# Kernel optimization log

Measured on AMD Instinct MI355X. Metric: run time of the kernel, lower is better.

The kernel has to match this reference:

```python
import jax, jax.numpy as jnp
import numpy as np

B, C, T, H, W = 4, 16, 32, 64, 64
KD = 2  # key_dim == value_dim == 2 (hard-coded by reshape in original)


def setup_inputs() -> dict:
    key = jax.random.key(0)
    k0, k1, k2, k3, k4 = jax.random.split(key, 5)
    hw = H * W
    x = jax.random.uniform(k0, (B, C, T, H, W), dtype=jnp.float32)
    # positive weights keep v and out_s*out_t positive so sqrt stays real
    w_qkv_s = jax.random.uniform(k1, (3 * KD, T), dtype=jnp.float32) * (2.0 / T)
    w_qkv_t = jax.random.uniform(k2, (3 * KD, hw), dtype=jnp.float32) * (2.0 / hw)
    w_out_s = jax.random.uniform(k3, (C, C * KD), dtype=jnp.float32) * (2.0 / (C * KD))
    w_out_t = jax.random.uniform(k4, (C, C * KD), dtype=jnp.float32) * (2.0 / (C * KD))
    return {"x": x, "w_qkv_s": w_qkv_s, "w_qkv_t": w_qkv_t,
            "w_out_s": w_out_s, "w_out_t": w_out_t}


def reference(x, w_qkv_s, w_qkv_t, w_out_s, w_out_t):
    b, c, t, h, w = x.shape
    hw = h * w
    # spatial qkv: 1x1 conv over time-as-channel -> (b,c,3*KD,hw)
    qkv_s = jnp.einsum('bcthw,kt->bckhw', x, w_qkv_s).reshape(b, c, 3 * KD, hw)
    qs, ks, vs = qkv_s[:, :, :KD], qkv_s[:, :, KD:2 * KD], qkv_s[:, :, 2 * KD:]
    # temporal qkv: 1x1 conv over space-as-channel -> (b,c,3*KD,t)
    x_flat = x.reshape(b, c, t, hw)
    qkv_t = jnp.einsum('bctn,kn->bckt', x_flat, w_qkv_t)
    qt, kt, vt = qkv_t[:, :, :KD], qkv_t[:, :, KD:2 * KD], qkv_t[:, :, 2 * KD:]

    qs = jax.nn.softmax(qs, axis=2)[:, :, :, None, :]   # (b,c,KD,1,hw)
    qt = jax.nn.softmax(qt, axis=2)[..., None]          # (b,c,KD,t,1)
    ks = jax.nn.softmax(ks, axis=-1)[:, :, :, None, :]  # (b,c,KD,1,hw)
    kt = jax.nn.softmax(kt, axis=-1)[..., None]         # (b,c,KD,t,1)
    vs = vs[:, :, :, None, :]
    vt = vt[..., None]

    eps = 1e-10
    scale = KD ** (-0.25)
    # log-space geometric mean of spatial and temporal maps -> (b,c,KD,t,hw)
    k = jnp.exp((jnp.log(kt + eps) + jnp.log(ks + eps)) * 0.5) * scale
    q = jnp.exp((jnp.log(qt + eps) + jnp.log(qs + eps)) * 0.5) * scale
    v = jnp.sqrt(vt * vs)

    context = jnp.einsum('bcdtn,bcetn->bcde', k, v)      # (b,c,KD,KD)
    out = jnp.einsum('bcdtn,bcde->bcetn', q, context)    # (b,c,KD,t,hw)
    out = out.reshape(b, c * KD, t, h, w)                # foldTime

    out_s = jnp.einsum('bkthw,ck->bcthw', out, w_out_s)
    out_t = jnp.einsum('bkthw,ck->bcthw', out, w_out_t)
    return jnp.sqrt(out_s * out_t)
```

## Files before the change

kernel.cpp:

```cpp
#include <hip/hip_runtime.h>

#define BB 4
#define CC 16
#define TT 32
#define HWN 4096
#define NCH1 16

#define WS_BQ   0
#define WS_QTP  (WS_BQ + BB*CC*2*HWN)
#define WS_KSP  (WS_QTP + BB*CC*NCH1*192)
#define WS_AQ   (WS_KSP + BB*CC*NCH1*8)
#define WS_CTX  (WS_AQ + BB*CC*2*TT)
#define WS_CST  (WS_CTX + BB*CC*2*2)

__device__ __forceinline__ float wsum64(float v){
#pragma unroll
  for (int m = 1; m < 64; m <<= 1) v += __shfl_xor(v, m, 64);
  return v;
}
__device__ __forceinline__ float wmax64(float v){
#pragma unroll
  for (int m = 1; m < 64; m <<= 1) v = fmaxf(v, __shfl_xor(v, m, 64));
  return v;
}
__device__ __forceinline__ float qsum4(float v){
  int a = __builtin_amdgcn_update_dpp(0, __float_as_int(v), 0xB1, 0xF, 0xF, true);
  float r = v + __int_as_float(a);
  int b = __builtin_amdgcn_update_dpp(0, __float_as_int(r), 0x4E, 0xF, 0xF, true);
  return r + __int_as_float(b);
}

__global__ __launch_bounds__(256) void k1_stage(const float* __restrict__ x,
    const float* __restrict__ wqs, const float* __restrict__ wqt,
    float* __restrict__ ws)
{
  const int bx = blockIdx.x;
  const int ch = bx & 15;
  const int c  = (bx >> 4) & 15;
  const int b  = bx >> 8;
  const int tid  = threadIdx.x;
  const int wave = tid >> 6;
  const int lane = tid & 63;
  const int wave_u = __builtin_amdgcn_readfirstlane(wave);

  __shared__ float4 sacc[4][64][6];
  __shared__ float  qred[4*836];

  const int n0 = ch*256 + lane*4;
  const float* xrow = x + (((size_t)(b*CC + c))*TT + wave_u*8)*(size_t)HWN + n0;

  float4 wt4[6];
#pragma unroll
  for (int k = 0; k < 6; ++k)
    wt4[k] = *(const float4*)(wqt + k*HWN + n0);

  float wq[6][8];
#pragma unroll
  for (int k = 0; k < 6; ++k)
#pragma unroll
    for (int tl = 0; tl < 8; ++tl)
      wq[k][tl] = wqs[k*TT + wave_u*8 + tl];

  float acc[6][4];
  float qt[6][8];
#pragma unroll
  for (int k = 0; k < 6; ++k){
#pragma unroll
    for (int j = 0; j < 4; ++j) acc[k][j] = 0.f;
#pragma unroll
    for (int tl = 0; tl < 8; ++tl) qt[k][tl] = 0.f;
  }

  float4 xv = *(const float4*)(xrow);
#pragma unroll
  for (int tl = 0; tl < 8; ++tl){
    float4 nxt = xv;
    if (tl < 7) nxt = *(const float4*)(xrow + (size_t)(tl+1)*HWN);
#pragma unroll
    for (int k = 0; k < 6; ++k){
      const float w = wq[k][tl];
      acc[k][0] = fmaf(xv.x, w, acc[k][0]);
      acc[k][1] = fmaf(xv.y, w, acc[k][1]);
      acc[k][2] = fmaf(xv.z, w, acc[k][2]);
      acc[k][3] = fmaf(xv.w, w, acc[k][3]);
      float p = qt[k][tl];
      p = fmaf(xv.x, wt4[k].x, p);
      p = fmaf(xv.y, wt4[k].y, p);
      p = fmaf(xv.z, wt4[k].z, p);
      p = fmaf(xv.w, wt4[k].w, p);
      qt[k][tl] = p;
    }
    xv = nxt;
  }

#pragma unroll
  for (int k = 0; k < 6; ++k)
#pragma unroll
    for (int tl = 0; tl < 8; ++tl)
      qt[k][tl] = qsum4(qt[k][tl]);
  if ((lane & 3) == 0){
    float* qp = &qred[wave*836 + (lane >> 2)*52];
#pragma unroll
    for (int k = 0; k < 6; ++k){
      *(float4*)(qp + k*8)     = make_float4(qt[k][0],qt[k][1],qt[k][2],qt[k][3]);
      *(float4*)(qp + k*8 + 4) = make_float4(qt[k][4],qt[k][5],qt[k][6],qt[k][7]);
    }
  }

#pragma unroll
  for (int k = 0; k < 6; ++k)
    sacc[wave][lane][k] = make_float4(acc[k][0], acc[k][1], acc[k][2], acc[k][3]);
  __syncthreads();

  const float eps = 1e-10f;

  if (tid < 192){
    const int k = tid >> 5, t = tid & 31, w = t >> 3, tl = t & 7;
    const float* qp = &qred[w*836 + k*8 + tl];
    float s = 0.f;
#pragma unroll
    for (int g = 0; g < 16; ++g) s += qp[g*52];
    ws[WS_QTP + ((size_t)((b*CC+c)*NCH1 + ch))*192 + tid] = s;
  }

  if (wave == 0){
    float4 s0 = sacc[0][lane][0], s1 = sacc[0][lane][1];
#pragma unroll
    for (int w = 1; w < 4; ++w){
      float4 a = sacc[w][lane][0], bq_ = sacc[w][lane][1];
      s0.x += a.x; s0.y += a.y; s0.z += a.z; s0.w += a.w;
      s1.x += bq_.x; s1.y += bq_.y; s1.z += bq_.z; s1.w += bq_.w;
    }
    float q0[4] = {s0.x, s0.y, s0.z, s0.w};
    float q1[4] = {s1.x, s1.y, s1.z, s1.w};
    float o0[4], o1[4];
#pragma unroll
    for (int j = 0; j < 4; ++j){
      float mm = fmaxf(q0[j], q1[j]);
      float e0 = __expf(q0[j]-mm), e1 = __expf(q1[j]-mm);
      float inv = 1.f/(e0+e1);
      o0[j] = sqrtf(e0*inv + eps);
      o1[j] = sqrtf(e1*inv + eps);
    }
    float* bqp = ws + WS_BQ + ((size_t)((b*CC+c)*2))*HWN + n0;
    *(float4*)(bqp)       = make_float4(o0[0],o0[1],o0[2],o0[3]);
    *(float4*)(bqp + HWN) = make_float4(o1[0],o1[1],o1[2],o1[3]);
  } else if (wave == 1){
    float4 ks0 = sacc[0][lane][2], ks1 = sacc[0][lane][3];
    float4 vs0 = sacc[0][lane][4], vs1 = sacc[0][lane][5];
#pragma unroll
    for (int w = 1; w < 4; ++w){
      float4 a = sacc[w][lane][2], bb = sacc[w][lane][3];
      float4 cc2 = sacc[w][lane][4], dd = sacc[w][lane][5];
      ks0.x += a.x; ks0.y += a.y; ks0.z += a.z; ks0.w += a.w;
      ks1.x += bb.x; ks1.y += bb.y; ks1.z += bb.z; ks1.w += bb.w;
      vs0.x += cc2.x; vs0.y += cc2.y; vs0.z += cc2.z; vs0.w += cc2.w;
      vs1.x += dd.x; vs1.y += dd.y; vs1.z += dd.z; vs1.w += dd.w;
    }
    float k0a[4] = {ks0.x,ks0.y,ks0.z,ks0.w};
    float k1a[4] = {ks1.x,ks1.y,ks1.z,ks1.w};
    float v0a[4] = {vs0.x,vs0.y,vs0.z,vs0.w};
    float v1a[4] = {vs1.x,vs1.y,vs1.z,vs1.w};
    float m0 = fmaxf(fmaxf(k0a[0],k0a[1]), fmaxf(k0a[2],k0a[3]));
    float m1 = fmaxf(fmaxf(k1a[0],k1a[1]), fmaxf(k1a[2],k1a[3]));
    m0 = wmax64(m0); m1 = wmax64(m1);
    float z0=0,z1=0,t00=0,t01=0,t10=0,t11=0;
#pragma unroll
    for (int j = 0; j < 4; ++j){
      float e0 = __expf(k0a[j]-m0);
      float e1 = __expf(k1a[j]-m1);
      z0 += e0; z1 += e1;
      float s0 = sqrtf(e0), s1 = sqrtf(e1);
      float v0 = sqrtf(v0a[j]), v1 = sqrtf(v1a[j]);
      t00 = fmaf(s0, v0, t00);
      t01 = fmaf(s1, v0, t01);
      t10 = fmaf(s0, v1, t10);
      t11 = fmaf(s1, v1, t11);
    }
    z0 = wsum64(z0); z1 = wsum64(z1);
    t00 = wsum64(t00); t01 = wsum64(t01); t10 = wsum64(t10); t11 = wsum64(t11);
    if (lane == 0){
      float* sp = ws + WS_KSP + ((size_t)((b*CC+c)*NCH1 + ch))*8;
      sp[0]=m0; sp[1]=m1; sp[2]=z0; sp[3]=z1;
      sp[4]=t00; sp[5]=t01; sp[6]=t10; sp[7]=t11;
    }
  }
}

__global__ __launch_bounds__(64) void k2_combine(float* __restrict__ ws)
{
  const int bc_ = blockIdx.x;
  const int tid = threadIdx.x;
  __shared__ float qt[192];
  const float eps = 1e-10f;
  const float scale = 0.8408964152537145f;

  for (int i = tid; i < 192; i += 64){
    float s = 0.f;
#pragma unroll
    for (int ch = 0; ch < NCH1; ++ch)
      s += ws[WS_QTP + ((size_t)(bc_*NCH1 + ch))*192 + i];
    qt[i] = s;
  }
  __syncthreads();

  if (tid < TT){
    const int t = tid;
    float q0 = qt[0*TT+t], q1 = qt[1*TT+t];
    float mm = fmaxf(q0,q1);
    float e0 = __expf(q0-mm), e1 = __expf(q1-mm);
    float inv = 1.f/(e0+e1);
    ws[WS_AQ + (bc_*2+0)*TT + t] = sqrtf(e0*inv + eps);
    ws[WS_AQ + (bc_*2+1)*TT + t] = sqrtf(e1*inv + eps);
  }
  if (tid < 2){
    const int d = tid;
    float M = -1e30f;
    for (int t = 0; t < TT; ++t) M = fmaxf(M, qt[(2+d)*TT+t]);
    float Z = 0.f;
    for (int t = 0; t < TT; ++t) Z += __expf(qt[(2+d)*TT+t]-M);
    const float invZ = 1.f/Z;
    float St0 = 0.f, St1 = 0.f;
    for (int t = 0; t < TT; ++t){
      float p = __expf(qt[(2+d)*TT+t]-M)*invZ;
      float r = sqrtf(p + eps);
      St0 += r*sqrtf(qt[4*TT+t]);
      St1 += r*sqrtf(qt[5*TT+t]);
    }
    const float* kp = ws + WS_KSP + (size_t)bc_*NCH1*8;
    float M2 = -1e30f;
    for (int ch = 0; ch < NCH1; ++ch) M2 = fmaxf(M2, kp[ch*8+d]);
    float Z2 = 0.f, Sn0 = 0.f, Sn1 = 0.f;
    for (int ch = 0; ch < NCH1; ++ch){
      const float mc = kp[ch*8+d];
      Z2  += kp[ch*8+2+d]*__expf(mc-M2);
      const float hw = __expf((mc-M2)*0.5f);
      Sn0 += kp[ch*8+4+d]*hw;
      Sn1 += kp[ch*8+6+d]*hw;
    }
    const float invsZ = rsqrtf(Z2);
    Sn0 *= invsZ; Sn1 *= invsZ;
    ws[WS_CTX + (bc_*2+d)*2+0] = scale*St0*Sn0;
    ws[WS_CTX + (bc_*2+d)*2+1] = scale*St1*Sn1;
  }
}

__global__ __launch_bounds__(64) void k3_cs(const float* __restrict__ wos,
    const float* __restrict__ wot, float* __restrict__ ws)
{
  const int bx = blockIdx.x;
  const int b = bx >> 5, t = bx & 31;
  const int tid = threadIdx.x;
  const int mat = tid >> 5, m = tid & 31;
  const int cp = m >> 1, d = m & 1;
  const float scale = 0.8408964152537145f;

  const float aq = ws[WS_AQ + ((size_t)((b*CC+cp)*2+d))*TT + t];
  const float c0 = ws[WS_CTX + ((b*CC+cp)*2+d)*2 + 0];
  const float c1 = ws[WS_CTX + ((b*CC+cp)*2+d)*2 + 1];
  const float a0 = scale*aq*c0, a1 = scale*aq*c1;
  const float* wmat = mat ? wot : wos;
  float vals[16];
#pragma unroll
  for (int c = 0; c < CC; ++c)
    vals[c] = fmaf(wmat[c*32 + cp*2], a0, wmat[c*32 + cp*2 + 1]*a1);
  float* dst = ws + WS_CST + (((size_t)(b*TT+t)*32 + m)*2 + mat)*16;
#pragma unroll
  for (int g = 0; g < 4; ++g)
    *(float4*)(dst + g*4) = make_float4(vals[g*4],vals[g*4+1],vals[g*4+2],vals[g*4+3]);
}

#define FMA4(acc, s, v) { acc.x = fmaf(s, v.x, acc.x); acc.y = fmaf(s, v.y, acc.y); \
                          acc.z = fmaf(s, v.z, acc.z); acc.w = fmaf(s, v.w, acc.w); }

__global__ __launch_bounds__(256) void k4_out(const float* __restrict__ ws,
    float* __restrict__ out)
{
  const int bx = blockIdx.x;
  const int nch  = bx & 3;
  const int half = (bx >> 2) & 1;
  const int t    = (bx >> 3) & (TT-1);
  const int b    = bx >> 8;
  const int tid  = threadIdx.x;

  const int n0 = nch*1024 + tid*4;
  const float* bqbase = ws + WS_BQ + ((size_t)(b*CC*2))*HWN + n0;
  const float* cst = ws + WS_CST + ((size_t)(b*TT+t))*1024 + half*8;

  float4 aS[8], aT[8];
#pragma unroll
  for (int c = 0; c < 8; ++c){
    aS[c] = make_float4(0,0,0,0);
    aT[c] = make_float4(0,0,0,0);
  }

#pragma unroll 4
  for (int m = 0; m < 32; ++m){
    const float4 bq = *(const float4*)(bqbase + (size_t)m*HWN);
    const float* cm = cst + m*32;
    const float4 cs0 = *(const float4*)(cm);
    const float4 cs1 = *(const float4*)(cm + 4);
    const float4 ct0 = *(const float4*)(cm + 16);
    const float4 ct1 = *(const float4*)(cm + 20);
    FMA4(aS[0], cs0.x, bq); FMA4(aS[1], cs0.y, bq);
    FMA4(aS[2], cs0.z, bq); FMA4(aS[3], cs0.w, bq);
    FMA4(aS[4], cs1.x, bq); FMA4(aS[5], cs1.y, bq);
    FMA4(aS[6], cs1.z, bq); FMA4(aS[7], cs1.w, bq);
    FMA4(aT[0], ct0.x, bq); FMA4(aT[1], ct0.y, bq);
    FMA4(aT[2], ct0.z, bq); FMA4(aT[3], ct0.w, bq);
    FMA4(aT[4], ct1.x, bq); FMA4(aT[5], ct1.y, bq);
    FMA4(aT[6], ct1.z, bq); FMA4(aT[7], ct1.w, bq);
  }

  float* outp = out + (((size_t)(b*CC + half*8))*TT + t)*HWN + n0;
#pragma unroll
  for (int c = 0; c < 8; ++c){
    float4 y;
    y.x = sqrtf(aS[c].x*aT[c].x);
    y.y = sqrtf(aS[c].y*aT[c].y);
    y.z = sqrtf(aS[c].z*aT[c].z);
    y.w = sqrtf(aS[c].w*aT[c].w);
    *(float4*)(outp + (size_t)c*TT*HWN) = y;
  }
}

extern "C" void kernel_launch(void* const* d_in, const int* in_sizes, int n_in,
                              void* d_out, int out_size, void* d_ws, size_t ws_size,
                              hipStream_t stream)
{
  const float* x   = (const float*)d_in[0];
  const float* wqs = (const float*)d_in[1];
  const float* wqt = (const float*)d_in[2];
  const float* wos = (const float*)d_in[3];
  const float* wot = (const float*)d_in[4];
  float* out = (float*)d_out;
  float* ws  = (float*)d_ws;

  hipLaunchKernelGGL(k1_stage, dim3(BB*CC*NCH1), dim3(256), 0, stream, x, wqs, wqt, ws);
  hipLaunchKernelGGL(k2_combine, dim3(BB*CC), dim3(64), 0, stream, ws);
  hipLaunchKernelGGL(k3_cs, dim3(BB*TT), dim3(64), 0, stream, wos, wot, ws);
  hipLaunchKernelGGL(k4_out, dim3(BB*TT*8), dim3(256), 0, stream, ws, out);
}
```

Before: 120.0 us.

## Fuse combine and coefficient kernels, halve per-thread width in output kernel

Merges the k2 combine and k3 coefficient kernels into one per-batch kernel that keeps intermediates (aq, context, output weights) in shared memory, saving a launch and a global round-trip. The output kernel now computes two pixels per thread instead of four, doubling the grid to 2048 blocks for more parallelism and lower register pressure. The fused kernel runs only 4 blocks, so its serial work per block grows, and the narrower output kernel reloads the coefficient table twice as often.

```diff
diff --git a/kernel.cpp b/kernel.cpp
--- a/kernel.cpp
+++ b/kernel.cpp
@@ -9,9 +9,7 @@
 #define WS_BQ   0
 #define WS_QTP  (WS_BQ + BB*CC*2*HWN)
 #define WS_KSP  (WS_QTP + BB*CC*NCH1*192)
-#define WS_AQ   (WS_KSP + BB*CC*NCH1*8)
-#define WS_CTX  (WS_AQ + BB*CC*2*TT)
-#define WS_CST  (WS_CTX + BB*CC*2*2)
+#define WS_CST  (WS_KSP + BB*CC*NCH1*8)
 
 __device__ __forceinline__ float wsum64(float v){
 #pragma unroll
@@ -187,47 +185,56 @@
   }
 }
 
-__global__ __launch_bounds__(64) void k2_combine(float* __restrict__ ws)
+__global__ __launch_bounds__(256) void k23_combine(const float* __restrict__ wos,
+    const float* __restrict__ wot, float* __restrict__ ws)
 {
-  const int bc_ = blockIdx.x;
+  const int b = blockIdx.x;
   const int tid = threadIdx.x;
-  __shared__ float qt[192];
+  __shared__ float qt_all[16][192];
+  __shared__ float aq[16][2][32];
+  __shared__ float ctxs[16][2][2];
+  __shared__ float wo[2][512];
   const float eps = 1e-10f;
-  const float scale = 0.8408964152537145f;
-
-  for (int i = tid; i < 192; i += 64){
+  const float scale2 = 0.7071067811865476f;
+
+  for (int i = tid; i < 512; i += 256){
+    wo[0][i] = wos[i];
+    wo[1][i] = wot[i];
+  }
+  for (int i = tid; i < 3072; i += 256){
+    const int c = i / 192, j = i - c*192;
+    const float* qp = ws + WS_QTP + ((size_t)((b*CC+c)*NCH1))*192 + j;
     float s = 0.f;
 #pragma unroll
-    for (int ch = 0; ch < NCH1; ++ch)
-      s += ws[WS_QTP + ((size_t)(bc_*NCH1 + ch))*192 + i];
-    qt[i] = s;
+    for (int ch = 0; ch < NCH1; ++ch) s += qp[ch*192];
+    qt_all[c][j] = s;
   }
   __syncthreads();
 
-  if (tid < TT){
-    const int t = tid;
-    float q0 = qt[0*TT+t], q1 = qt[1*TT+t];
+  for (int i = tid; i < 512; i += 256){
+    const int c = i >> 5, t = i & 31;
+    float q0 = qt_all[c][t], q1 = qt_all[c][32+t];
     float mm = fmaxf(q0,q1);
     float e0 = __expf(q0-mm), e1 = __expf(q1-mm);
     float inv = 1.f/(e0+e1);
-    ws[WS_AQ + (bc_*2+0)*TT + t] = sqrtf(e0*inv + eps);
-    ws[WS_AQ + (bc_*2+1)*TT + t] = sqrtf(e1*inv + eps);
-  }
-  if (tid < 2){
-    const int d = tid;
+    aq[c][0][t] = sqrtf(e0*inv + eps);
+    aq[c][1][t] = sqrtf(e1*inv + eps);
+  }
+  if (tid < 32){
+    const int c = tid >> 1, d = tid & 1;
+    const float* kt = &qt_all[c][(2+d)*32];
     float M = -1e30f;
-    for (int t = 0; t < TT; ++t) M = fmaxf(M, qt[(2+d)*TT+t]);
+    for (int t = 0; t < TT; ++t) M = fmaxf(M, kt[t]);
     float Z = 0.f;
-    for (int t = 0; t < TT; ++t) Z += __expf(qt[(2+d)*TT+t]-M);
+    for (int t = 0; t < TT; ++t) Z += __expf(kt[t]-M);
     const float invZ = 1.f/Z;
     float St0 = 0.f, St1 = 0.f;
     for (int t = 0; t < TT; ++t){
-      float p = __expf(qt[(2+d)*TT+t]-M)*invZ;
-      float r = sqrtf(p + eps);
-      St0 += r*sqrtf(qt[4*TT+t]);
-      St1 += r*sqrtf(qt[5*TT+t]);
-    }
-    const float* kp = ws + WS_KSP + (size_t)bc_*NCH1*8;
+      float r = sqrtf(__expf(kt[t]-M)*invZ + eps);
+      St0 += r*sqrtf(qt_all[c][128+t]);
+      St1 += r*sqrtf(qt_all[c][160+t]);
+    }
+    const float* kp = ws + WS_KSP + ((size_t)(b*CC+c))*NCH1*8;
     float M2 = -1e30f;
     for (int ch = 0; ch < NCH1; ++ch) M2 = fmaxf(M2, kp[ch*8+d]);
     float Z2 = 0.f, Sn0 = 0.f, Sn1 = 0.f;
@@ -239,88 +246,75 @@
       Sn1 += kp[ch*8+6+d]*hw;
     }
     const float invsZ = rsqrtf(Z2);
-    Sn0 *= invsZ; Sn1 *= invsZ;
-    ws[WS_CTX + (bc_*2+d)*2+0] = scale*St0*Sn0;
-    ws[WS_CTX + (bc_*2+d)*2+1] = scale*St1*Sn1;
-  }
-}
-
-__global__ __launch_bounds__(64) void k3_cs(const float* __restrict__ wos,
-    const float* __restrict__ wot, float* __restrict__ ws)
-{
-  const int bx = blockIdx.x;
-  const int b = bx >> 5, t = bx & 31;
-  const int tid = threadIdx.x;
-  const int mat = tid >> 5, m = tid & 31;
-  const int cp = m >> 1, d = m & 1;
-  const float scale = 0.8408964152537145f;
-
-  const float aq = ws[WS_AQ + ((size_t)((b*CC+cp)*2+d))*TT + t];
-  const float c0 = ws[WS_CTX + ((b*CC+cp)*2+d)*2 + 0];
-  const float c1 = ws[WS_CTX + ((b*CC+cp)*2+d)*2 + 1];
-  const float a0 = scale*aq*c0, a1 = scale*aq*c1;
-  const float* wmat = mat ? wot : wos;
-  float vals[16];
-#pragma unroll
-  for (int c = 0; c < CC; ++c)
-    vals[c] = fmaf(wmat[c*32 + cp*2], a0, wmat[c*32 + cp*2 + 1]*a1);
-  float* dst = ws + WS_CST + (((size_t)(b*TT+t)*32 + m)*2 + mat)*16;
-#pragma unroll
-  for (int g = 0; g < 4; ++g)
-    *(float4*)(dst + g*4) = make_float4(vals[g*4],vals[g*4+1],vals[g*4+2],vals[g*4+3]);
-}
-
-#define FMA4(acc, s, v) { acc.x = fmaf(s, v.x, acc.x); acc.y = fmaf(s, v.y, acc.y); \
-                          acc.z = fmaf(s, v.z, acc.z); acc.w = fmaf(s, v.w, acc.w); }
+    ctxs[c][d][0] = scale2*St0*Sn0*invsZ;
+    ctxs[c][d][1] = scale2*St1*Sn1*invsZ;
+  }
+  __syncthreads();
+
+  for (int i = tid; i < 2048; i += 256){
+    const int t = i >> 6, rem = i & 63, mat = rem >> 5, m = rem & 31;
+    const int cp = m >> 1, d = m & 1;
+    const float a  = aq[cp][d][t];
+    const float a0 = a*ctxs[cp][d][0], a1 = a*ctxs[cp][d][1];
+    float vals[16];
+#pragma unroll
+    for (int c = 0; c < CC; ++c)
+      vals[c] = fmaf(wo[mat][c*32 + cp*2], a0, wo[mat][c*32 + cp*2 + 1]*a1);
+    float* dst = ws + WS_CST + ((size_t)(b*TT+t))*1024 + m*32 + mat*16;
+#pragma unroll
+    for (int g = 0; g < 4; ++g)
+      *(float4*)(dst + g*4) = make_float4(vals[g*4],vals[g*4+1],vals[g*4+2],vals[g*4+3]);
+  }
+}
+
+#define FMA2(acc, s, v) { acc.x = fmaf(s, v.x, acc.x); acc.y = fmaf(s, v.y, acc.y); }
 
 __global__ __launch_bounds__(256) void k4_out(const float* __restrict__ ws,
     float* __restrict__ out)
 {
   const int bx = blockIdx.x;
-  const int nch  = bx & 3;
-  const int half = (bx >> 2) & 1;
-  const int t    = (bx >> 3) & (TT-1);
-  const int b    = bx >> 8;
+  const int nch  = bx & 7;
+  const int half = (bx >> 3) & 1;
+  const int t    = (bx >> 4) & (TT-1);
+  const int b    = bx >> 9;
   const int tid  = threadIdx.x;
 
-  const int n0 = nch*1024 + tid*4;
+  const int n0 = nch*512 + tid*2;
   const float* bqbase = ws + WS_BQ + ((size_t)(b*CC*2))*HWN + n0;
   const float* cst = ws + WS_CST + ((size_t)(b*TT+t))*1024 + half*8;
 
-  float4 aS[8], aT[8];
+  float2 aS[8], aT[8];
 #pragma unroll
   for (int c = 0; c < 8; ++c){
-    aS[c] = make_float4(0,0,0,0);
-    aT[c] = make_float4(0,0,0,0);
-  }
-
-#pragma unroll 4
+    aS[c] = make_float2(0.f,0.f);
+    aT[c] = make_float2(0.f,0.f);
+  }
+
+#pragma unroll 8
   for (int m = 0; m < 32; ++m){
-    const float4 bq = *(const float4*)(bqbase + (size_t)m*HWN);
+    const float2 bq = *(const float2*)(bqbase + (size_t)m*HWN);
     const float* cm = cst + m*32;
     const float4 cs0 = *(const float4*)(cm);
     const float4 cs1 = *(const float4*)(cm + 4);
     const float4 ct0 = *(const float4*)(cm + 16);
     const float4 ct1 = *(const float4*)(cm + 20);
-    FMA4(aS[0], cs0.x, bq); FMA4(aS[1], cs0.y, bq);
-    FMA4(aS[2], cs0.z, bq); FMA4(aS[3], cs0.w, bq);
-    FMA4(aS[4], cs1.x, bq); FMA4(aS[5], cs1.y, bq);
-    FMA4(aS[6], cs1.z, bq); FMA4(aS[7], cs1.w, bq);
-    FMA4(aT[0], ct0.x, bq); FMA4(aT[1], ct0.y, bq);
-    FMA4(aT[2], ct0.z, bq); FMA4(aT[3], ct0.w, bq);
-    FMA4(aT[4], ct1.x, bq); FMA4(aT[5], ct1.y, bq);
-    FMA4(aT[6], ct1.z, bq); FMA4(aT[7], ct1.w, bq);
+    FMA2(aS[0], cs0.x, bq); FMA2(aS[1], cs0.y, bq);
+    FMA2(aS[2], cs0.z, bq); FMA2(aS[3], cs0.w, bq);
+    FMA2(aS[4], cs1.x, bq); FMA2(aS[5], cs1.y, bq);
+    FMA2(aS[6], cs1.z, bq); FMA2(aS[7], cs1.w, bq);
+    FMA2(aT[0], ct0.x, bq); FMA2(aT[1], ct0.y, bq);
+    FMA2(aT[2], ct0.z, bq); FMA2(aT[3], ct0.w, bq);
+    FMA2(aT[4], ct1.x, bq); FMA2(aT[5], ct1.y, bq);
+    FMA2(aT[6], ct1.z, bq); FMA2(aT[7], ct1.w, bq);
   }
 
   float* outp = out + (((size_t)(b*CC + half*8))*TT + t)*HWN + n0;
 #pragma unroll
   for (int c = 0; c < 8; ++c){
-    float4 y;
+    float2 y;
     y.x = sqrtf(aS[c].x*aT[c].x);
     y.y = sqrtf(aS[c].y*aT[c].y);
-    y.z = sqrtf(aS[c].z*aT[c].z);
-    y.w = sqrtf(aS[c].w*aT[c].w);
-    *(float4*)(outp + (size_t)c*TT*HWN) = y;
+    *(float2*)(outp + (size_t)c*TT*HWN) = y;
   }
 }
 
@@ -337,7 +331,6 @@
   float* ws  = (float*)d_ws;
 
   hipLaunchKernelGGL(k1_stage, dim3(BB*CC*NCH1), dim3(256), 0, stream, x, wqs, wqt, ws);
-  hipLaunchKernelGGL(k2_combine, dim3(BB*CC), dim3(64), 0, stream, ws);
-  hipLaunchKernelGGL(k3_cs, dim3(BB*TT), dim3(64), 0, stream, wos, wot, ws);
-  hipLaunchKernelGGL(k4_out, dim3(BB*TT*8), dim3(256), 0, stream, ws, out);
-}
+  hipLaunchKernelGGL(k23_combine, dim3(BB), dim3(256), 0, stream, wos, wot, ws);
+  hipLaunchKernelGGL(k4_out, dim3(BB*TT*2*8), dim3(256), 0, stream, ws, out);
+}
```

Result: slower. 131.2 us (+9.3%).
